# Kernel optimization log

Measured on AMD Instinct MI355X. Metric: run time of the kernel, lower is better.

Reference implementation:

```python
import jax, jax.numpy as jnp
import numpy as np

ROPE_BASE = 10000.0


def _apply_rope(q, k, start_pos):
    # q, k: (B, T, H, D) with half-split (LLaMA-style) rotation
    B, T, H, D = q.shape
    half = D // 2
    inv_freq = 1.0 / (ROPE_BASE ** (jnp.arange(0, half, dtype=jnp.float32) / half))
    pos = (start_pos + jnp.arange(T)).astype(jnp.float32)
    ang = pos[:, None] * inv_freq[None, :]          # (T, half)
    cos = jnp.cos(ang)[None, :, None, :]            # (1, T, 1, half)
    sin = jnp.sin(ang)[None, :, None, :]

    def rot(t):
        t1, t2 = t[..., :half], t[..., half:]
        return jnp.concatenate([t1 * cos - t2 * sin, t1 * sin + t2 * cos], axis=-1)

    return rot(q), rot(k)


def setup_inputs() -> dict:
    key = jax.random.key(0)
    k1, k2, k3 = jax.random.split(key, 3)
    B, T, C = 2, 2048, 2048
    x = jax.random.normal(k1, (B, T, C), dtype=jnp.float32)
    # torch Linear weights: (out_features, in_features), scaled like default init
    Wqkv = jax.random.normal(k2, (3 * C, C), dtype=jnp.float32) * (C ** -0.5)
    Wproj = jax.random.normal(k3, (C, C), dtype=jnp.float32) * (C ** -0.5)
    return {"x": x, "Wqkv": Wqkv, "Wproj": Wproj, "start_pos": 0}


def reference(x, Wqkv, Wproj, start_pos):
    B, T, C = x.shape
    H = 16
    D = C // H
    scale = D ** -0.5

    qkv = x @ Wqkv.T                                 # (B, T, 3C)
    q, k, v = jnp.split(qkv, 3, axis=-1)
    q = q.reshape(B, T, H, D)
    k = k.reshape(B, T, H, D)
    v = v.reshape(B, T, H, D)
    q, k = _apply_rope(q, k, start_pos)

    att = jnp.einsum("bthd,bshd->bhts", q, k) * scale   # (B, H, T, T)
    causal = jnp.tril(jnp.ones((T, T), dtype=bool))
    att = jnp.where(causal[None, None], att, -jnp.inf)
    att = jax.nn.softmax(att, axis=-1)
    out = jnp.einsum("bhts,bshd->bthd", att, v)          # (B, T, H, D)
    out = out.reshape(B, T, C)
    return out @ Wproj.T
```

## Files before the change

### kernel.cpp

```cpp
#include <hip/hip_runtime.h>
#include <hip/hip_bf16.h>
#include <stdint.h>
#include <math.h>

#define B_    2
#define T_    2048
#define C_    2048
#define H_    16
#define D_    128
#define NQKV  6144
#define BT_   4096

typedef __attribute__((ext_vector_type(8))) short  short8;
typedef __attribute__((ext_vector_type(4))) short  short4_;
typedef __attribute__((ext_vector_type(4))) float  float4_;

__device__ __forceinline__ unsigned short f2bf(float f) {
  union { float f; unsigned int u; } v; v.f = f;
  unsigned int u = v.u;
  return (unsigned short)((u + 0x7FFFu + ((u >> 16) & 1u)) >> 16);
}
__device__ __forceinline__ float bf2f(unsigned short u) {
  union { unsigned int i; float f; } v; v.i = ((unsigned int)u) << 16;
  return v.f;
}
__device__ __forceinline__ void pk2(short4_& dst, int idx2, float a, float b) {
  union { __hip_bfloat162 h2; struct { short x, y; } s; } u;
  u.h2 = __float22bfloat162_rn(make_float2(a, b));
  dst[idx2 * 2]     = u.s.x;
  dst[idx2 * 2 + 1] = u.s.y;
}

__device__ __forceinline__ void async_cp16(const unsigned short* g, unsigned short* l) {
  __builtin_amdgcn_global_load_lds((__attribute__((address_space(1))) void*)g,
                                   (__attribute__((address_space(3))) void*)l,
                                   16, 0, 0);
}

__global__ __launch_bounds__(256) void cvt_bf16(const float* __restrict__ in,
                                                unsigned short* __restrict__ out, int n) {
  int i = (blockIdx.x * 256 + threadIdx.x) * 8;
  if (i + 8 > n) return;
  const float4_* p = (const float4_*)(in + i);
  float4_ a = p[0], b = p[1];
  short8 o;
  o[0] = (short)f2bf(a[0]); o[1] = (short)f2bf(a[1]);
  o[2] = (short)f2bf(a[2]); o[3] = (short)f2bf(a[3]);
  o[4] = (short)f2bf(b[0]); o[5] = (short)f2bf(b[1]);
  o[6] = (short)f2bf(b[2]); o[7] = (short)f2bf(b[3]);
  *(short8*)(out + i) = o;
}

template <bool F32OUT>
__global__ __launch_bounds__(256) void gemm_bt(const unsigned short* __restrict__ A,
                                               const unsigned short* __restrict__ Bm,
                                               void* __restrict__ Cout,
                                               int M, int N, int K) {
  __shared__ __align__(16) unsigned short As[128 * 64];
  __shared__ __align__(16) unsigned short Bs[128 * 64];
  const int tid  = threadIdx.x;
  const int lane = tid & 63;
  const int col16 = lane & 15, quad = lane >> 4;
  const int wave = tid >> 6;
  const int wm = wave >> 1, wn = wave & 1;
  const int m0 = blockIdx.y * 128, n0 = blockIdx.x * 128;

  float4_ acc[4][4] = {};

  #pragma unroll 1
  for (int k0 = 0; k0 < K; k0 += 64) {
    __syncthreads();
    #pragma unroll
    for (int i = 0; i < 4; ++i) {
      int P   = i * 256 + tid;
      int row = P >> 3;
      int kc  = (P & 7) ^ (row & 7);
      async_cp16(A  + (size_t)(m0 + row) * K + k0 + kc * 8, As + P * 8);
      async_cp16(Bm + (size_t)(n0 + row) * K + k0 + kc * 8, Bs + P * 8);
    }
    __syncthreads();
    #pragma unroll
    for (int ks = 0; ks < 2; ++ks) {
      short8 af[4], bf[4];
      #pragma unroll
      for (int i = 0; i < 4; ++i) {
        int ra = wm * 64 + i * 16 + col16;
        int ca = ((ks * 4 + quad) ^ (ra & 7)) * 8;
        af[i] = *(const short8*)(As + ra * 64 + ca);
        int rb = wn * 64 + i * 16 + col16;
        int cb = ((ks * 4 + quad) ^ (rb & 7)) * 8;
        bf[i] = *(const short8*)(Bs + rb * 64 + cb);
      }
      #pragma unroll
      for (int i = 0; i < 4; ++i)
        #pragma unroll
        for (int j = 0; j < 4; ++j)
          acc[i][j] = __builtin_amdgcn_mfma_f32_16x16x32_bf16(af[i], bf[j], acc[i][j], 0, 0, 0);
    }
  }

  #pragma unroll
  for (int i = 0; i < 4; ++i) {
    int mg = m0 + wm * 64 + i * 16 + quad * 4;
    #pragma unroll
    for (int j = 0; j < 4; ++j) {
      int ng = n0 + wn * 64 + j * 16 + col16;
      #pragma unroll
      for (int r = 0; r < 4; ++r) {
        if constexpr (F32OUT)
          ((float*)Cout)[(size_t)(mg + r) * N + ng] = acc[i][j][r];
        else
          ((unsigned short*)Cout)[(size_t)(mg + r) * N + ng] = f2bf(acc[i][j][r]);
      }
    }
  }
}

__global__ __launch_bounds__(256) void rope_split(const unsigned short* __restrict__ qkv,
                                                  const int* __restrict__ sp_ptr,
                                                  unsigned short* __restrict__ q_r,
                                                  unsigned short* __restrict__ k_r,
                                                  unsigned short* __restrict__ v_t) {
  __shared__ __align__(16) unsigned short vs[128 * 64];
  const int blk  = blockIdx.x;
  const int bh   = blk >> 5;
  const int tile = blk & 31;
  const int b = bh >> 4, h = bh & 15;
  const int t0 = tile * 64;
  const int tid = threadIdx.x;
  const int qidx = tid & 15;
  const int sp = sp_ptr[0];
  const bool hi = (qidx & 8) != 0;
  const float L2F = -0.20762050593046013f;
  const float SCL = 0.1275174117f;

  #pragma unroll
  for (int p = 0; p < 4; ++p) {
    int row = p * 16 + (tid >> 4);
    int tg  = t0 + row;
    size_t base = (size_t)(b * T_ + tg) * NQKV + h * D_ + qidx * 8;
    short8 q8 = *(const short8*)(qkv + base);
    short8 k8 = *(const short8*)(qkv + base + 2048);
    short8 v8 = *(const short8*)(qkv + base + 4096);
    float qf[8], kf[8], qp[8], kp[8];
    #pragma unroll
    for (int j = 0; j < 8; ++j) { qf[j] = bf2f((unsigned short)q8[j]); kf[j] = bf2f((unsigned short)k8[j]); }
    #pragma unroll
    for (int j = 0; j < 8; ++j) { qp[j] = __shfl_xor(qf[j], 8); kp[j] = __shfl_xor(kf[j], 8); }
    float pos = (float)(sp + tg);
    short8 qo, ko;
    #pragma unroll
    for (int j = 0; j < 8; ++j) {
      int d  = qidx * 8 + j;
      int fi = d & 63;
      float freq = exp2f((float)fi * L2F);
      float ang = pos * freq;
      float s = sinf(ang), c = cosf(ang);
      float sq = s * SCL, cq = c * SCL;
      float o1 = hi ? (qp[j] * sq + qf[j] * cq) : (qf[j] * cq - qp[j] * sq);
      float o2 = hi ? (kp[j] * s  + kf[j] * c ) : (kf[j] * c  - kp[j] * s );
      qo[j] = (short)f2bf(o1);
      ko[j] = (short)f2bf(o2);
    }
    size_t ob = (size_t)(bh * T_ + tg) * D_ + qidx * 8;
    *(short8*)(q_r + ob) = qo;
    *(short8*)(k_r + ob) = ko;
    #pragma unroll
    for (int j = 0; j < 8; ++j) {
      int d  = qidx * 8 + j;
      int prc = (row >> 3) ^ ((d >> 3) & 7);
      vs[d * 64 + prc * 8 + (row & 7)] = (unsigned short)v8[j];
    }
  }
  __syncthreads();
  int drow = tid >> 1;
  int half = tid & 1;
  size_t gb = (size_t)(bh * D_ + drow) * T_ + t0 + half * 32;
  #pragma unroll
  for (int c = 0; c < 4; ++c) {
    int rc  = half * 4 + c;
    int prc = rc ^ ((drow >> 3) & 7);
    *(short8*)(v_t + gb + c * 8) = *(const short8*)(vs + drow * 64 + prc * 8);
  }
}

__global__ __launch_bounds__(256) void attn_fwd(const unsigned short* __restrict__ q_r,
                                                const unsigned short* __restrict__ k_r,
                                                const unsigned short* __restrict__ v_t,
                                                unsigned short* __restrict__ Ob) {
  __shared__ __align__(16) unsigned short Ks[2][64 * 128];
  __shared__ __align__(16) unsigned short Vts[2][128 * 64];
  __shared__ __align__(16) unsigned short Ps[64 * 64];
  const int pairb = blockIdx.x;
  const int bh    = blockIdx.y;
  const int tid  = threadIdx.x;
  const int lane = tid & 63;
  const int col16 = lane & 15, quad = lane >> 4;
  const int wave = tid >> 6;
  const float NEG_INF = -__builtin_inff();
  const int b = bh >> 4, h = bh & 15;
  const int qlr = wave * 16 + col16;

  #pragma unroll 1
  for (int half = 0; half < 2; ++half) {
    const int qt = half ? (31 - pairb) : pairb;
    const int q0 = qt * 64;

    short8 qf[4];
    const unsigned short* qp = q_r + (size_t)(bh * T_ + q0 + qlr) * D_;
    #pragma unroll
    for (int ks = 0; ks < 4; ++ks) qf[ks] = *(const short8*)(qp + ks * 32 + quad * 8);

    float4_ oacc[8] = {};
    float m_i = NEG_INF, l_i = 0.f;

    __syncthreads();

    const unsigned short* kbase = k_r + (size_t)bh * T_ * D_;
    const unsigned short* vbase = v_t + (size_t)bh * D_ * T_;
    #define STAGE(JT, BUF)                                                        \
      {                                                                           \
        const unsigned short* kb = kbase + (size_t)(JT) * 64 * D_;                \
        const unsigned short* vb = vbase + (size_t)(JT) * 64;                     \
        unsigned short* kd = &Ks[(BUF)][0];                                       \
        unsigned short* vd = &Vts[(BUF)][0];                                      \
        _Pragma("unroll")                                                         \
        for (int i = 0; i < 4; ++i) {                                             \
          int P = i * 256 + tid;                                                  \
          int krow = P >> 4, kc = (P & 15) ^ (krow & 7);                          \
          async_cp16(kb + krow * D_ + kc * 8, kd + P * 8);                        \
          int vrow = P >> 3, vc = (P & 7) ^ (vrow & 7);                           \
          async_cp16(vb + (size_t)vrow * T_ + vc * 8, vd + P * 8);                \
        }                                                                         \
      }

    STAGE(0, 0);

    #pragma unroll 1
    for (int jt = 0; jt <= qt; ++jt) {
      __syncthreads();
      if (jt < qt) STAGE(jt + 1, (jt + 1) & 1);
      const unsigned short* KsB  = &Ks[jt & 1][0];
      const unsigned short* VtsB = &Vts[jt & 1][0];

      float4_ s[4];
      #pragma unroll
      for (int jn = 0; jn < 4; ++jn) {
        float4_ a = {};
        #pragma unroll
        for (int ks = 0; ks < 4; ++ks) {
          int kr = jn * 16 + col16;
          int ch = ((ks * 4 + quad) ^ (kr & 7)) * 8;
          short8 kfr = *(const short8*)(KsB + kr * 128 + ch);
          a = __builtin_amdgcn_mfma_f32_16x16x32_bf16(kfr, qf[ks], a, 0, 0, 0);
        }
        s[jn] = a;
      }
      if (jt == qt) {
        #pragma unroll
        for (int jn = 0; jn < 4; ++jn)
          #pragma unroll
          for (int r = 0; r < 4; ++r)
            if (jn * 16 + quad * 4 + r > qlr) s[jn][r] = NEG_INF;
      }
      float rm = NEG_INF;
      #pragma unroll
      for (int jn = 0; jn < 4; ++jn)
        #pragma unroll
        for (int r = 0; r < 4; ++r) rm = fmaxf(rm, s[jn][r]);
      rm = fmaxf(rm, __shfl_xor(rm, 16));
      rm = fmaxf(rm, __shfl_xor(rm, 32));
      float m_new = fmaxf(m_i, rm);
      float alpha = exp2f(m_i - m_new);
      float rs = 0.f;
      #pragma unroll
      for (int jn = 0; jn < 4; ++jn)
        #pragma unroll
        for (int r = 0; r < 4; ++r) {
          float pv = exp2f(s[jn][r] - m_new);
          s[jn][r] = pv;
          rs += pv;
        }
      rs += __shfl_xor(rs, 16);
      rs += __shfl_xor(rs, 32);
      l_i = l_i * alpha + rs;
      m_i = m_new;
      #pragma unroll
      for (int dt = 0; dt < 8; ++dt) oacc[dt] *= alpha;

      #pragma unroll
      for (int jn = 0; jn < 4; ++jn) {
        short4_ pkv;
        pk2(pkv, 0, s[jn][0], s[jn][1]);
        pk2(pkv, 1, s[jn][2], s[jn][3]);
        int c0 = jn * 16 + quad * 4;
        int ch = (c0 >> 3) ^ (qlr & 7);
        *(short4_*)(Ps + qlr * 64 + ch * 8 + (c0 & 7)) = pkv;
      }
      __builtin_amdgcn_s_waitcnt(0xC07F);

      short8 pf[2];
      #pragma unroll
      for (int ks2 = 0; ks2 < 2; ++ks2) {
        int ch = ((ks2 * 4 + quad) ^ (qlr & 7)) * 8;
        pf[ks2] = *(const short8*)(Ps + qlr * 64 + ch);
      }
      #pragma unroll
      for (int dt = 0; dt < 8; ++dt)
        #pragma unroll
        for (int ks2 = 0; ks2 < 2; ++ks2) {
          int vr = dt * 16 + col16;
          int ch = ((ks2 * 4 + quad) ^ (vr & 7)) * 8;
          short8 vf = *(const short8*)(VtsB + vr * 64 + ch);
          oacc[dt] = __builtin_amdgcn_mfma_f32_16x16x32_bf16(vf, pf[ks2], oacc[dt], 0, 0, 0);
        }
    }

    float inv_l = 1.0f / l_i;
    size_t ob = (size_t)(b * T_ + q0 + qlr) * C_ + h * D_;
    #pragma unroll
    for (int dt = 0; dt < 8; ++dt) {
      short4_ o4;
      pk2(o4, 0, oacc[dt][0] * inv_l, oacc[dt][1] * inv_l);
      pk2(o4, 1, oacc[dt][2] * inv_l, oacc[dt][3] * inv_l);
      *(short4_*)(Ob + ob + dt * 16 + quad * 4) = o4;
    }
    #undef STAGE
  }
}

extern "C" void kernel_launch(void* const* d_in, const int* in_sizes, int n_in,
                              void* d_out, int out_size, void* d_ws, size_t ws_size,
                              hipStream_t stream) {
  const float* x     = (const float*)d_in[0];
  const float* Wqkv  = (const float*)d_in[1];
  const float* Wproj = (const float*)d_in[2];
  const int*   sp    = (const int*)d_in[3];
  float* out = (float*)d_out;

  unsigned short* ws     = (unsigned short*)d_ws;
  unsigned short* xb     = ws;
  unsigned short* wqkvb  = xb + 8388608;
  unsigned short* wprojb = wqkvb + 12582912;
  unsigned short* qkvb   = wprojb + 4194304;
  unsigned short* q_r    = qkvb + 25165824;
  unsigned short* k_r    = q_r + 8388608;
  unsigned short* v_t    = k_r + 8388608;
  unsigned short* Obuf   = xb;

  cvt_bf16<<<8388608 / 2048, 256, 0, stream>>>(x, xb, 8388608);
  cvt_bf16<<<12582912 / 2048, 256, 0, stream>>>(Wqkv, wqkvb, 12582912);
  cvt_bf16<<<4194304 / 2048, 256, 0, stream>>>(Wproj, wprojb, 4194304);

  gemm_bt<false><<<dim3(48, 32), 256, 0, stream>>>(xb, wqkvb, (void*)qkvb, BT_, NQKV, C_);

  rope_split<<<1024, 256, 0, stream>>>(qkvb, sp, q_r, k_r, v_t);

  attn_fwd<<<dim3(16, 32), 256, 0, stream>>>(q_r, k_r, v_t, Obuf);

  gemm_bt<true><<<dim3(16, 32), 256, 0, stream>>>(Obuf, wprojb, (void*)out, BT_, C_, C_);
}
```

Measured before the change: 395.9 us.

## Use 128-row query tiles with 8 waves in attention and fuse bf16 conversions

The attention kernel now runs 512 threads per block, and each block handles a 128-query tile, so every staged K/V tile in shared memory is reused by twice as many query rows. Waves skip fully masked key tiles, and the causal mask is applied per wave at diagonal tiles. The grid is flattened to 256 blocks with bh as the fast index, and the three fp32-to-bf16 conversion launches are merged into one kernel. The changes reduce K/V staging traffic and launch overhead, but per-wave work is unbalanced on diagonal tiles and the grid has fewer blocks.

Result: faster. 384.2 us (-3.0%).

```diff
diff --git a/kernel.cpp b/kernel.cpp
--- a/kernel.cpp
+++ b/kernel.cpp
@@ -37,11 +37,16 @@
                                    16, 0, 0);
 }
 
-__global__ __launch_bounds__(256) void cvt_bf16(const float* __restrict__ in,
-                                                unsigned short* __restrict__ out, int n) {
+__global__ __launch_bounds__(256) void cvt_all(const float* __restrict__ x,
+                                               const float* __restrict__ wqkv,
+                                               const float* __restrict__ wproj,
+                                               unsigned short* __restrict__ out) {
   int i = (blockIdx.x * 256 + threadIdx.x) * 8;
-  if (i + 8 > n) return;
-  const float4_* p = (const float4_*)(in + i);
+  const float* src; int off;
+  if (i < 8388608)       { src = x;     off = i; }
+  else if (i < 20971520) { src = wqkv;  off = i - 8388608; }
+  else                   { src = wproj; off = i - 20971520; }
+  const float4_* p = (const float4_*)(src + off);
   float4_ a = p[0], b = p[1];
   short8 o;
   o[0] = (short)f2bf(a[0]); o[1] = (short)f2bf(a[1]);
@@ -184,15 +189,15 @@
   }
 }
 
-__global__ __launch_bounds__(256) void attn_fwd(const unsigned short* __restrict__ q_r,
+__global__ __launch_bounds__(512) void attn_fwd(const unsigned short* __restrict__ q_r,
                                                 const unsigned short* __restrict__ k_r,
                                                 const unsigned short* __restrict__ v_t,
                                                 unsigned short* __restrict__ Ob) {
   __shared__ __align__(16) unsigned short Ks[2][64 * 128];
   __shared__ __align__(16) unsigned short Vts[2][128 * 64];
-  __shared__ __align__(16) unsigned short Ps[64 * 64];
-  const int pairb = blockIdx.x;
-  const int bh    = blockIdx.y;
+  __shared__ __align__(16) unsigned short Ps[128 * 64];
+  const int pairb = blockIdx.x >> 5;
+  const int bh    = blockIdx.x & 31;
   const int tid  = threadIdx.x;
   const int lane = tid & 63;
   const int col16 = lane & 15, quad = lane >> 4;
@@ -203,8 +208,9 @@
 
   #pragma unroll 1
   for (int half = 0; half < 2; ++half) {
-    const int qt = half ? (31 - pairb) : pairb;
-    const int q0 = qt * 64;
+    const int qt = half ? (15 - pairb) : pairb;
+    const int q0 = qt * 128;
+    const int njt = 2 * qt + 2;
 
     short8 qf[4];
     const unsigned short* qp = q_r + (size_t)(bh * T_ + q0 + qlr) * D_;
@@ -225,8 +231,8 @@
         unsigned short* kd = &Ks[(BUF)][0];                                       \
         unsigned short* vd = &Vts[(BUF)][0];                                      \
         _Pragma("unroll")                                                         \
-        for (int i = 0; i < 4; ++i) {                                             \
-          int P = i * 256 + tid;                                                  \
+        for (int i = 0; i < 2; ++i) {                                             \
+          int P = i * 512 + tid;                                                  \
           int krow = P >> 4, kc = (P & 15) ^ (krow & 7);                          \
           async_cp16(kb + krow * D_ + kc * 8, kd + P * 8);                        \
           int vrow = P >> 3, vc = (P & 7) ^ (vrow & 7);                           \
@@ -237,9 +243,12 @@
     STAGE(0, 0);
 
     #pragma unroll 1
-    for (int jt = 0; jt <= qt; ++jt) {
+    for (int jt = 0; jt < njt; ++jt) {
       __syncthreads();
-      if (jt < qt) STAGE(jt + 1, (jt + 1) & 1);
+      if (jt + 1 < njt) STAGE(jt + 1, (jt + 1) & 1);
+
+      if (jt * 64 > q0 + wave * 16 + 15) continue;
+
       const unsigned short* KsB  = &Ks[jt & 1][0];
       const unsigned short* VtsB = &Vts[jt & 1][0];
 
@@ -256,12 +265,12 @@
         }
         s[jn] = a;
       }
-      if (jt == qt) {
+      if (jt * 64 + 63 > q0 + wave * 16) {
         #pragma unroll
         for (int jn = 0; jn < 4; ++jn)
           #pragma unroll
           for (int r = 0; r < 4; ++r)
-            if (jn * 16 + quad * 4 + r > qlr) s[jn][r] = NEG_INF;
+            if (jt * 64 + jn * 16 + quad * 4 + r > q0 + qlr) s[jn][r] = NEG_INF;
       }
       float rm = NEG_INF;
       #pragma unroll
@@ -348,15 +357,13 @@
   unsigned short* v_t    = k_r + 8388608;
   unsigned short* Obuf   = xb;
 
-  cvt_bf16<<<8388608 / 2048, 256, 0, stream>>>(x, xb, 8388608);
-  cvt_bf16<<<12582912 / 2048, 256, 0, stream>>>(Wqkv, wqkvb, 12582912);
-  cvt_bf16<<<4194304 / 2048, 256, 0, stream>>>(Wproj, wprojb, 4194304);
+  cvt_all<<<25165824 / 2048, 256, 0, stream>>>(x, Wqkv, Wproj, ws);
 
   gemm_bt<false><<<dim3(48, 32), 256, 0, stream>>>(xb, wqkvb, (void*)qkvb, BT_, NQKV, C_);
 
   rope_split<<<1024, 256, 0, stream>>>(qkvb, sp, q_r, k_r, v_t);
 
-  attn_fwd<<<dim3(16, 32), 256, 0, stream>>>(q_r, k_r, v_t, Obuf);
+  attn_fwd<<<dim3(256), 512, 0, stream>>>(q_r, k_r, v_t, Obuf);
 
   gemm_bt<true><<<dim3(16, 32), 256, 0, stream>>>(Obuf, wprojb, (void*)out, BT_, C_, C_);
 }
```
